# Kernel tuning notes

Measured on AMD Instinct MI355X. Metric: run time of the kernel, lower is better.

## Reference

```python
import jax, jax.numpy as jnp
import numpy as np

RADIUS = 0.12   # init_kwargs radius
NSAMPLE = 32    # init_kwargs nsample
USE_XYZ = True  # init_kwargs use_xyz


def ball_query(xyz, new_xyz, radius, nsample):
    """xyz: (B,N,3), new_xyz: (B,M,3) -> idx (B,M,nsample) int32.
    PointNet++ semantics: first `nsample` points (in index order) within
    `radius` of each query; slots past the count are padded with the first
    found index."""
    B, N, _ = xyz.shape
    # squared distances (B, M, N) -- the dominant intermediate
    d2 = jnp.sum((new_xyz[:, :, None, :] - xyz[:, None, :, :]) ** 2, axis=-1)
    mask = d2 < radius * radius
    # score so that earlier in-ball indices have higher score; out-of-ball = 0
    score = jnp.where(mask, (N - jnp.arange(N, dtype=jnp.int32)), 0)
    _, idx = jax.lax.top_k(score, nsample)            # (B, M, nsample)
    valid = jnp.take_along_axis(mask, idx, axis=-1)   # which slots are real hits
    idx = jnp.where(valid, idx, idx[..., :1])         # pad with first found index
    return idx


def group_points(feat, idx):
    """feat: (B,C,N), idx: (B,M,S) -> (B,C,M,S) gather along N."""
    B, C, N = feat.shape
    M, S = idx.shape[1], idx.shape[2]
    idx_flat = jnp.broadcast_to(idx.reshape(B, 1, M * S), (B, C, M * S))
    out = jnp.take_along_axis(feat, idx_flat, axis=2)
    return out.reshape(B, C, M, S)


def setup_inputs() -> dict:
    key = jax.random.key(0)
    k1, k2 = jax.random.split(key)
    B, N, M, C = 4, 8192, 4096, 64
    xyz = jax.random.uniform(k1, (B, N, 3), dtype=jnp.float32)  # points in unit cube
    new_xyz = xyz[:, :M, :]                                      # FPS-like subset of points
    features = jax.random.normal(k2, (B, C, N), dtype=jnp.float32)
    return {"xyz": xyz, "new_xyz": new_xyz, "features": features}


def reference(xyz, new_xyz, features):
    idx = ball_query(xyz, new_xyz, RADIUS, NSAMPLE)             # (B,M,S)
    xyz_t = jnp.transpose(xyz, (0, 2, 1))                        # (B,3,N)
    grouped_xyz = group_points(xyz_t, idx)                       # (B,3,M,S)
    grouped_xyz = grouped_xyz - jnp.transpose(new_xyz, (0, 2, 1))[..., None]
    grouped_feat = group_points(features, idx)                   # (B,C,M,S)
    if USE_XYZ:
        new_features = jnp.concatenate([grouped_xyz, grouped_feat], axis=1)
    else:
        new_features = grouped_feat
    return new_features  # (B, 3+C, M, S)
```

## Files before the change

kernel.cpp:

```cpp
#include <hip/hip_runtime.h>
#include <cstdint>
#include <cstddef>

#define BB 4
#define NN 8192
#define MM 4096
#define CC 64
#define SS 32
#define CH 67
#define NC 512
#define RMARG 0.1201f

__device__ __constant__ float kRR = (float)(0.12 * 0.12);

__device__ __forceinline__ int cell_of(float x, float y, float z) {
    const int ix = min((int)(x * 8.0f), 7);
    const int iy = min((int)(y * 8.0f), 7);
    const int iz = min((int)(z * 8.0f), 7);
    return (ix << 6) + (iy << 3) + iz;
}

__device__ __forceinline__ int block_scan512(int v, int tid, int* wsum) {
    int incl = v;
    #pragma unroll
    for (int d = 1; d < 64; d <<= 1) {
        const int t = __shfl_up(incl, d);
        if ((tid & 63) >= d) incl += t;
    }
    if ((tid & 63) == 63 && tid < NC) wsum[tid >> 6] = incl;
    __syncthreads();
    if (tid < 8) {
        const int ws = wsum[tid];
        int w2 = ws;
        #pragma unroll
        for (int d = 1; d < 8; d <<= 1) {
            const int t = __shfl_up(w2, d);
            if (tid >= d) w2 += t;
        }
        wsum[tid] = w2 - ws;
    }
    __syncthreads();
    return incl + wsum[(tid >> 6) & 7];
}

__global__ __launch_bounds__(1024) void k_prep(
    const float* __restrict__ xyz,
    const float* __restrict__ new_xyz,
    const float* __restrict__ feat,
    float* __restrict__ ft,
    int* __restrict__ cellStart,
    int* __restrict__ qperm,
    float4* __restrict__ pk)
{
    __shared__ __align__(16) char smem[64 * 65 * sizeof(float)];
    const int blk = (int)blockIdx.x;
    const int tid = (int)threadIdx.x;

    if (blk < BB) {
        int* sm   = (int*)smem;
        int* cur  = sm + NC;
        int* wsum = cur + NC;
        const int b = blk;

        if (tid < NC) sm[tid] = 0;
        __syncthreads();

        float xs[8], ys[8], zs[8];
        int cl[8];
        const float* __restrict__ xb = xyz + (size_t)b * NN * 3;
        #pragma unroll
        for (int k = 0; k < 8; ++k) {
            const int n = (k << 10) + tid;
            xs[k] = xb[n * 3 + 0];
            ys[k] = xb[n * 3 + 1];
            zs[k] = xb[n * 3 + 2];
            cl[k] = cell_of(xs[k], ys[k], zs[k]);
            atomicAdd(&sm[cl[k]], 1);
        }
        __syncthreads();

        const int v = (tid < NC) ? sm[tid] : 0;
        const int incl = block_scan512(v, tid, wsum);
        if (tid < NC) {
            cellStart[b * (NC + 1) + tid + 1] = incl;
            cur[tid] = incl - v;
            if (tid == 0) cellStart[b * (NC + 1)] = 0;
        }
        __syncthreads();

        #pragma unroll
        for (int k = 0; k < 8; ++k) {
            const int n = (k << 10) + tid;
            const int pos = atomicAdd(&cur[cl[k]], 1);
            pk[b * NN + pos] = make_float4(xs[k], ys[k], zs[k], __int_as_float(n));
        }
        __syncthreads();

        if (tid < NC) sm[tid] = 0;
        __syncthreads();
        int qcl[4];
        const float* __restrict__ qb = new_xyz + (size_t)b * MM * 3;
        #pragma unroll
        for (int k = 0; k < 4; ++k) {
            const int qm = (k << 10) + tid;
            const float qx = qb[qm * 3 + 0];
            const float qy = qb[qm * 3 + 1];
            const float qz = qb[qm * 3 + 2];
            qcl[k] = cell_of(qx, qy, qz);
            atomicAdd(&sm[qcl[k]], 1);
        }
        __syncthreads();
        const int qv = (tid < NC) ? sm[tid] : 0;
        const int qincl = block_scan512(qv, tid, wsum);
        if (tid < NC) cur[tid] = qincl - qv;
        __syncthreads();
        #pragma unroll
        for (int k = 0; k < 4; ++k) {
            const int qm = (k << 10) + tid;
            const int pos = atomicAdd(&cur[qcl[k]], 1);
            qperm[b * MM + pos] = qm;
        }
    } else {
        float (*tile)[65] = (float(*)[65])smem;
        const int blk2 = blk - BB;
        const int b = blk2 / (NN / 64);
        const int n0 = (blk2 % (NN / 64)) * 64;
        const int tn = tid & 63;
        const int q = tid >> 6;
        const float* __restrict__ fb = feat + (size_t)b * CC * NN;
        #pragma unroll
        for (int k = 0; k < 4; ++k) {
            const int c = (q << 2) + k;
            tile[tn][c] = fb[(size_t)c * NN + n0 + tn];
        }
        __syncthreads();
        float* fo = ft + ((size_t)b * NN + n0) * CC;
        #pragma unroll
        for (int k = 0; k < 4; ++k) {
            const int rn = (q << 2) + k;
            fo[(size_t)rn * CC + tn] = tile[rn][tn];
        }
    }
}

__global__ __launch_bounds__(256) void qg_grid_kernel(
    const float4* __restrict__ pk,
    const int* __restrict__ cellStart,
    const int* __restrict__ qperm,
    const float* __restrict__ ft,
    const float* __restrict__ xyz,
    const float* __restrict__ new_xyz,
    float* __restrict__ out)
{
    __shared__ unsigned int bm[4][NN / 32];
    __shared__ int slots_sm[4][SS];

    const int tid = (int)threadIdx.x;
    const int lane = tid & 63;
    const int w = tid >> 6;
    const int wave = (int)blockIdx.x * 4 + w;
    const int b = wave >> 12;
    const int msort = wave & (MM - 1);
    const int m = qperm[b * MM + msort];

    unsigned int* __restrict__ bitmap = bm[w];
    int* __restrict__ slot = slots_sm[w];

    #pragma unroll
    for (int k = 0; k < 4; ++k) bitmap[(k << 6) + lane] = 0u;

    const float* __restrict__ xb = xyz + (size_t)b * NN * 3;
    const size_t qoff = ((size_t)b * MM + m) * 3;
    const float cx = new_xyz[qoff + 0];
    const float cy = new_xyz[qoff + 1];
    const float cz = new_xyz[qoff + 2];
    const float rr = kRR;

    const int x0 = max(0, (int)((cx - RMARG) * 8.0f));
    const int x1 = min(7, (int)((cx + RMARG) * 8.0f));
    const int y0 = max(0, (int)((cy - RMARG) * 8.0f));
    const int y1 = min(7, (int)((cy + RMARG) * 8.0f));
    const int z0 = max(0, (int)((cz - RMARG) * 8.0f));
    const int z1 = min(7, (int)((cz + RMARG) * 8.0f));

    const int* __restrict__ cs = cellStart + b * (NC + 1);
    const float4* __restrict__ pb = pk + b * NN;

    const int ny = y1 - y0 + 1;
    const int npair = (x1 - x0 + 1) * ny;
    int begL = 0, endL = 0;
    if (lane < npair) {
        const int px = lane / ny;
        const int py = lane - px * ny;
        const int cb2 = ((x0 + px) << 6) + ((y0 + py) << 3);
        begL = cs[cb2 + z0];
        endL = cs[cb2 + z1 + 1];
    }

    for (int p = 0; p < npair; ++p) {
        const int beg = __shfl(begL, p);
        const int end = __shfl(endL, p);
        for (int off = beg; off < end; off += 64) {
            const int a = off + lane;
            const bool act = a < end;
            const float4 v = pb[act ? a : beg];
            const float dx = __fsub_rn(v.x, cx);
            const float dy = __fsub_rn(v.y, cy);
            const float dz = __fsub_rn(v.z, cz);
            const float d2 = __fadd_rn(__fadd_rn(__fmul_rn(dx, dx), __fmul_rn(dy, dy)),
                                       __fmul_rn(dz, dz));
            if (act && d2 < rr) {
                const int n = __float_as_int(v.w);
                atomicOr(&bitmap[n >> 5], 1u << (n & 31));
            }
        }
    }

    const uint4 wv = *reinterpret_cast<const uint4*>(&bitmap[lane << 2]);
    const int pc = __popc(wv.x) + __popc(wv.y) + __popc(wv.z) + __popc(wv.w);
    int incl = pc;
    #pragma unroll
    for (int d = 1; d < 64; d <<= 1) {
        const int t = __shfl_up(incl, d);
        if (lane >= d) incl += t;
    }
    const int K = __shfl(incl, 63);
    int r = incl - pc;
    if (r < SS) {
        const int base = lane << 7;
        unsigned int mw0 = wv.x, mw1 = wv.y, mw2 = wv.z, mw3 = wv.w;
        while (mw0 && r < SS) { slot[r++] = base +  0 + __builtin_ctz(mw0); mw0 &= mw0 - 1; }
        while (mw1 && r < SS) { slot[r++] = base + 32 + __builtin_ctz(mw1); mw1 &= mw1 - 1; }
        while (mw2 && r < SS) { slot[r++] = base + 64 + __builtin_ctz(mw2); mw2 &= mw2 - 1; }
        while (mw3 && r < SS) { slot[r++] = base + 96 + __builtin_ctz(mw3); mw3 &= mw3 - 1; }
    }

    const int s = lane & 31;
    const int h = lane >> 5;
    const int Kc = (K < SS) ? K : SS;
    int n_of;
    if (Kc == 0) n_of = 0;
    else n_of = (s < Kc) ? slot[s] : slot[0];

    const size_t obase = ((size_t)b * CH) * (size_t)(MM * SS) + (size_t)m * SS + s;

    if (h == 0) {
        const float* xr = xb + (size_t)n_of * 3;
        __builtin_nontemporal_store(__fsub_rn(xr[0], cx), &out[obase + 0 * (size_t)(MM * SS)]);
        __builtin_nontemporal_store(__fsub_rn(xr[1], cy), &out[obase + 1 * (size_t)(MM * SS)]);
        __builtin_nontemporal_store(__fsub_rn(xr[2], cz), &out[obase + 2 * (size_t)(MM * SS)]);
    }
    const float4* fr4 = (const float4*)(ft + ((size_t)b * NN + n_of) * CC + (h << 5));
    float4 f[8];
    #pragma unroll
    for (int j = 0; j < 8; ++j) f[j] = fr4[j];
    #pragma unroll
    for (int j = 0; j < 8; ++j) {
        float* cb = &out[obase + (size_t)(3 + (h << 5) + (j << 2)) * (size_t)(MM * SS)];
        __builtin_nontemporal_store(f[j].x, cb + 0 * (size_t)(MM * SS));
        __builtin_nontemporal_store(f[j].y, cb + 1 * (size_t)(MM * SS));
        __builtin_nontemporal_store(f[j].z, cb + 2 * (size_t)(MM * SS));
        __builtin_nontemporal_store(f[j].w, cb + 3 * (size_t)(MM * SS));
    }
}

__global__ __launch_bounds__(256) void qg_fused_kernel(
    const float* __restrict__ xyz, const float* __restrict__ new_xyz,
    const float* __restrict__ feat, float* __restrict__ out)
{
    const int wave = (int)((blockIdx.x * blockDim.x + threadIdx.x) >> 6);
    const int lane = (int)(threadIdx.x & 63);
    const int b = wave / MM;
    const int m = wave % MM;

    const float* __restrict__ xb = xyz + (size_t)b * NN * 3;
    const size_t qoff = ((size_t)b * MM + m) * 3;
    const float cx = new_xyz[qoff + 0];
    const float cy = new_xyz[qoff + 1];
    const float cz = new_xyz[qoff + 2];
    const float rr = kRR;

    int my_nb = -1;
    int cnt = 0;

    for (int base = 0; base < NN; base += 512) {
        float px[8], py[8], pz[8];
        #pragma unroll
        for (int k = 0; k < 8; ++k) {
            const int i = base + (k << 6) + lane;
            px[k] = xb[i * 3 + 0]; py[k] = xb[i * 3 + 1]; pz[k] = xb[i * 3 + 2];
        }
        #pragma unroll
        for (int k = 0; k < 8; ++k) {
            const float dx = __fsub_rn(px[k], cx);
            const float dy = __fsub_rn(py[k], cy);
            const float dz = __fsub_rn(pz[k], cz);
            const float d2 = __fadd_rn(__fadd_rn(__fmul_rn(dx, dx), __fmul_rn(dy, dy)),
                                       __fmul_rn(dz, dz));
            const bool hit = d2 < rr;
            const unsigned long long mask = __ballot(hit);
            const int pc = __popcll(mask);
            if (pc) {
                const int rank = cnt + (int)__popcll(mask & ((1ull << lane) - 1ull));
                const int addr = (hit && rank < 63) ? rank : 63;
                const int recv = __builtin_amdgcn_ds_permute(addr << 2,
                                                             base + (k << 6) + lane);
                if (lane >= cnt && lane < SS && (lane - cnt) < pc) my_nb = recv;
                cnt += pc;
                if (cnt >= SS) break;
            }
        }
        if (cnt >= SS) break;
    }

    int first = __shfl(my_nb, 0);
    if (first < 0) first = 0;
    if (lane < SS && my_nb < 0) my_nb = first;
    const int n_of = __shfl(my_nb, lane & 31);

    const int s = lane & 31;
    const int h = lane >> 5;
    const size_t obase = ((size_t)b * CH) * (size_t)(MM * SS) + (size_t)m * SS + s;
    const float* __restrict__ fb = feat + (size_t)b * CC * NN;
    #pragma unroll 2
    for (int cc = 0; cc < CH + 1; cc += 2) {
        const int c = cc + h;
        if (c < CH) {
            float v;
            if (c < 3) {
                const float center = (c == 0) ? cx : (c == 1) ? cy : cz;
                v = __fsub_rn(xb[(size_t)n_of * 3 + c], center);
            } else {
                v = fb[(size_t)(c - 3) * NN + n_of];
            }
            out[obase + (size_t)c * (size_t)(MM * SS)] = v;
        }
    }
}

extern "C" void kernel_launch(void* const* d_in, const int* in_sizes, int n_in,
                              void* d_out, int out_size, void* d_ws, size_t ws_size,
                              hipStream_t stream) {
    const float* xyz     = (const float*)d_in[0];
    const float* new_xyz = (const float*)d_in[1];
    const float* feat    = (const float*)d_in[2];
    float* out = (float*)d_out;

    const size_t ft_b = (size_t)BB * NN * CC * sizeof(float);
    float*  ft     = (float*)d_ws;
    int*    cellSt = (int*)((char*)d_ws + ft_b);
    int*    qperm  = cellSt + BB * (NC + 1);
    char*   after  = (char*)(qperm + BB * MM);
    float4* pk     = (float4*)(((uintptr_t)after + 15) & ~(uintptr_t)15);
    const size_t need = ((char*)(pk + BB * NN) - (char*)d_ws);

    if (ws_size >= need) {
        k_prep<<<BB + BB * (NN / 64), 1024, 0, stream>>>(xyz, new_xyz, feat, ft,
                                                         cellSt, qperm, pk);
        qg_grid_kernel<<<(BB * MM) / 4, 256, 0, stream>>>(pk, cellSt, qperm, ft,
                                                          xyz, new_xyz, out);
    } else {
        qg_fused_kernel<<<(BB * MM) / 4, 256, 0, stream>>>(xyz, new_xyz, feat, out);
    }
}
```

Baseline: 57.34 us.

## Process two consecutive queries per wave and drop query cell-sort permutation

Each wave now handles two adjacent queries in sequence, building a bitmap per query, then all 64 lanes write 64 contiguous output slots (two queries × 32 samples) per channel plane. This makes stores fully coalesced at 256 bytes per plane instead of 128. The qperm spatial sort of queries in the prep kernel is removed, so queries are processed in natural index order. The cost is half as many waves, each with serialized neighbor search, plus loss of spatial locality from the sort, which may increase divergence and cache misses.

```diff
diff --git a/kernel.cpp b/kernel.cpp
--- a/kernel.cpp
+++ b/kernel.cpp
@@ -45,11 +45,9 @@
 
 __global__ __launch_bounds__(1024) void k_prep(
     const float* __restrict__ xyz,
-    const float* __restrict__ new_xyz,
     const float* __restrict__ feat,
     float* __restrict__ ft,
     int* __restrict__ cellStart,
-    int* __restrict__ qperm,
     float4* __restrict__ pk)
 {
     __shared__ __align__(16) char smem[64 * 65 * sizeof(float)];
@@ -93,32 +91,6 @@
             const int n = (k << 10) + tid;
             const int pos = atomicAdd(&cur[cl[k]], 1);
             pk[b * NN + pos] = make_float4(xs[k], ys[k], zs[k], __int_as_float(n));
-        }
-        __syncthreads();
-
-        if (tid < NC) sm[tid] = 0;
-        __syncthreads();
-        int qcl[4];
-        const float* __restrict__ qb = new_xyz + (size_t)b * MM * 3;
-        #pragma unroll
-        for (int k = 0; k < 4; ++k) {
-            const int qm = (k << 10) + tid;
-            const float qx = qb[qm * 3 + 0];
-            const float qy = qb[qm * 3 + 1];
-            const float qz = qb[qm * 3 + 2];
-            qcl[k] = cell_of(qx, qy, qz);
-            atomicAdd(&sm[qcl[k]], 1);
-        }
-        __syncthreads();
-        const int qv = (tid < NC) ? sm[tid] : 0;
-        const int qincl = block_scan512(qv, tid, wsum);
-        if (tid < NC) cur[tid] = qincl - qv;
-        __syncthreads();
-        #pragma unroll
-        for (int k = 0; k < 4; ++k) {
-            const int qm = (k << 10) + tid;
-            const int pos = atomicAdd(&cur[qcl[k]], 1);
-            qperm[b * MM + pos] = qm;
         }
     } else {
         float (*tile)[65] = (float(*)[65])smem;
@@ -146,121 +118,133 @@
 __global__ __launch_bounds__(256) void qg_grid_kernel(
     const float4* __restrict__ pk,
     const int* __restrict__ cellStart,
-    const int* __restrict__ qperm,
     const float* __restrict__ ft,
     const float* __restrict__ xyz,
     const float* __restrict__ new_xyz,
     float* __restrict__ out)
 {
-    __shared__ unsigned int bm[4][NN / 32];
-    __shared__ int slots_sm[4][SS];
+    __shared__ unsigned int bm[4][2][NN / 32];
+    __shared__ int slots_sm[4][2][SS];
 
     const int tid = (int)threadIdx.x;
     const int lane = tid & 63;
     const int w = tid >> 6;
-    const int wave = (int)blockIdx.x * 4 + w;
-    const int b = wave >> 12;
-    const int msort = wave & (MM - 1);
-    const int m = qperm[b * MM + msort];
-
-    unsigned int* __restrict__ bitmap = bm[w];
-    int* __restrict__ slot = slots_sm[w];
+    const int pair = (int)blockIdx.x * 4 + w;
+    const int b = pair >> 11;
+    const int m0 = (pair & 2047) << 1;
 
     #pragma unroll
-    for (int k = 0; k < 4; ++k) bitmap[(k << 6) + lane] = 0u;
+    for (int k = 0; k < 8; ++k) bm[w][k & 1][((k >> 1) << 6) + lane] = 0u;
 
     const float* __restrict__ xb = xyz + (size_t)b * NN * 3;
-    const size_t qoff = ((size_t)b * MM + m) * 3;
-    const float cx = new_xyz[qoff + 0];
-    const float cy = new_xyz[qoff + 1];
-    const float cz = new_xyz[qoff + 2];
+    const float* __restrict__ qb = new_xyz + ((size_t)b * MM + m0) * 3;
+    const float cxq[2] = { qb[0], qb[3] };
+    const float cyq[2] = { qb[1], qb[4] };
+    const float czq[2] = { qb[2], qb[5] };
     const float rr = kRR;
-
-    const int x0 = max(0, (int)((cx - RMARG) * 8.0f));
-    const int x1 = min(7, (int)((cx + RMARG) * 8.0f));
-    const int y0 = max(0, (int)((cy - RMARG) * 8.0f));
-    const int y1 = min(7, (int)((cy + RMARG) * 8.0f));
-    const int z0 = max(0, (int)((cz - RMARG) * 8.0f));
-    const int z1 = min(7, (int)((cz + RMARG) * 8.0f));
 
     const int* __restrict__ cs = cellStart + b * (NC + 1);
     const float4* __restrict__ pb = pk + b * NN;
 
-    const int ny = y1 - y0 + 1;
-    const int npair = (x1 - x0 + 1) * ny;
-    int begL = 0, endL = 0;
-    if (lane < npair) {
-        const int px = lane / ny;
-        const int py = lane - px * ny;
-        const int cb2 = ((x0 + px) << 6) + ((y0 + py) << 3);
-        begL = cs[cb2 + z0];
-        endL = cs[cb2 + z1 + 1];
-    }
-
-    for (int p = 0; p < npair; ++p) {
-        const int beg = __shfl(begL, p);
-        const int end = __shfl(endL, p);
-        for (int off = beg; off < end; off += 64) {
-            const int a = off + lane;
-            const bool act = a < end;
-            const float4 v = pb[act ? a : beg];
-            const float dx = __fsub_rn(v.x, cx);
-            const float dy = __fsub_rn(v.y, cy);
-            const float dz = __fsub_rn(v.z, cz);
-            const float d2 = __fadd_rn(__fadd_rn(__fmul_rn(dx, dx), __fmul_rn(dy, dy)),
-                                       __fmul_rn(dz, dz));
-            if (act && d2 < rr) {
-                const int n = __float_as_int(v.w);
-                atomicOr(&bitmap[n >> 5], 1u << (n & 31));
+    int Kcq[2];
+
+    #pragma unroll
+    for (int q = 0; q < 2; ++q) {
+        const float cx = cxq[q], cy = cyq[q], cz = czq[q];
+        unsigned int* __restrict__ bitmap = bm[w][q];
+        int* __restrict__ slot = slots_sm[w][q];
+
+        const int x0 = max(0, (int)((cx - RMARG) * 8.0f));
+        const int x1 = min(7, (int)((cx + RMARG) * 8.0f));
+        const int y0 = max(0, (int)((cy - RMARG) * 8.0f));
+        const int y1 = min(7, (int)((cy + RMARG) * 8.0f));
+        const int z0 = max(0, (int)((cz - RMARG) * 8.0f));
+        const int z1 = min(7, (int)((cz + RMARG) * 8.0f));
+
+        const int ny = y1 - y0 + 1;
+        const int npair = (x1 - x0 + 1) * ny;
+        int begL = 0, endL = 0;
+        if (lane < npair) {
+            const int px = lane / ny;
+            const int py = lane - px * ny;
+            const int cb2 = ((x0 + px) << 6) + ((y0 + py) << 3);
+            begL = cs[cb2 + z0];
+            endL = cs[cb2 + z1 + 1];
+        }
+
+        for (int p = 0; p < npair; ++p) {
+            const int beg = __shfl(begL, p);
+            const int end = __shfl(endL, p);
+            for (int off = beg; off < end; off += 64) {
+                const int a = off + lane;
+                const bool act = a < end;
+                const float4 v = pb[act ? a : beg];
+                const float dx = __fsub_rn(v.x, cx);
+                const float dy = __fsub_rn(v.y, cy);
+                const float dz = __fsub_rn(v.z, cz);
+                const float d2 = __fadd_rn(__fadd_rn(__fmul_rn(dx, dx), __fmul_rn(dy, dy)),
+                                           __fmul_rn(dz, dz));
+                if (act && d2 < rr) {
+                    const int n = __float_as_int(v.w);
+                    atomicOr(&bitmap[n >> 5], 1u << (n & 31));
+                }
             }
         }
-    }
-
-    const uint4 wv = *reinterpret_cast<const uint4*>(&bitmap[lane << 2]);
-    const int pc = __popc(wv.x) + __popc(wv.y) + __popc(wv.z) + __popc(wv.w);
-    int incl = pc;
-    #pragma unroll
-    for (int d = 1; d < 64; d <<= 1) {
-        const int t = __shfl_up(incl, d);
-        if (lane >= d) incl += t;
-    }
-    const int K = __shfl(incl, 63);
-    int r = incl - pc;
-    if (r < SS) {
-        const int base = lane << 7;
-        unsigned int mw0 = wv.x, mw1 = wv.y, mw2 = wv.z, mw3 = wv.w;
-        while (mw0 && r < SS) { slot[r++] = base +  0 + __builtin_ctz(mw0); mw0 &= mw0 - 1; }
-        while (mw1 && r < SS) { slot[r++] = base + 32 + __builtin_ctz(mw1); mw1 &= mw1 - 1; }
-        while (mw2 && r < SS) { slot[r++] = base + 64 + __builtin_ctz(mw2); mw2 &= mw2 - 1; }
-        while (mw3 && r < SS) { slot[r++] = base + 96 + __builtin_ctz(mw3); mw3 &= mw3 - 1; }
-    }
-
+
+        const uint4 wv = *reinterpret_cast<const uint4*>(&bitmap[lane << 2]);
+        const int pc = __popc(wv.x) + __popc(wv.y) + __popc(wv.z) + __popc(wv.w);
+        int incl = pc;
+        #pragma unroll
+        for (int d = 1; d < 64; d <<= 1) {
+            const int t = __shfl_up(incl, d);
+            if (lane >= d) incl += t;
+        }
+        const int K = __shfl(incl, 63);
+        int r = incl - pc;
+        if (r < SS) {
+            const int base = lane << 7;
+            unsigned int mw0 = wv.x, mw1 = wv.y, mw2 = wv.z, mw3 = wv.w;
+            while (mw0 && r < SS) { slot[r++] = base +  0 + __builtin_ctz(mw0); mw0 &= mw0 - 1; }
+            while (mw1 && r < SS) { slot[r++] = base + 32 + __builtin_ctz(mw1); mw1 &= mw1 - 1; }
+            while (mw2 && r < SS) { slot[r++] = base + 64 + __builtin_ctz(mw2); mw2 &= mw2 - 1; }
+            while (mw3 && r < SS) { slot[r++] = base + 96 + __builtin_ctz(mw3); mw3 &= mw3 - 1; }
+        }
+        Kcq[q] = (K < SS) ? K : SS;
+    }
+
+    const int q = lane >> 5;
     const int s = lane & 31;
-    const int h = lane >> 5;
-    const int Kc = (K < SS) ? K : SS;
+    const int Kc = q ? Kcq[1] : Kcq[0];
     int n_of;
     if (Kc == 0) n_of = 0;
-    else n_of = (s < Kc) ? slot[s] : slot[0];
-
-    const size_t obase = ((size_t)b * CH) * (size_t)(MM * SS) + (size_t)m * SS + s;
-
-    if (h == 0) {
+    else n_of = slots_sm[w][q][(s < Kc) ? s : 0];
+
+    const size_t plane = (size_t)(MM * SS);
+    const size_t obase = ((size_t)b * CH) * plane + (size_t)m0 * SS + lane;
+
+    {
         const float* xr = xb + (size_t)n_of * 3;
-        __builtin_nontemporal_store(__fsub_rn(xr[0], cx), &out[obase + 0 * (size_t)(MM * SS)]);
-        __builtin_nontemporal_store(__fsub_rn(xr[1], cy), &out[obase + 1 * (size_t)(MM * SS)]);
-        __builtin_nontemporal_store(__fsub_rn(xr[2], cz), &out[obase + 2 * (size_t)(MM * SS)]);
-    }
-    const float4* fr4 = (const float4*)(ft + ((size_t)b * NN + n_of) * CC + (h << 5));
-    float4 f[8];
+        const float gx = __fsub_rn(xr[0], q ? cxq[1] : cxq[0]);
+        const float gy = __fsub_rn(xr[1], q ? cyq[1] : cyq[0]);
+        const float gz = __fsub_rn(xr[2], q ? czq[1] : czq[0]);
+        __builtin_nontemporal_store(gx, &out[obase + 0 * plane]);
+        __builtin_nontemporal_store(gy, &out[obase + 1 * plane]);
+        __builtin_nontemporal_store(gz, &out[obase + 2 * plane]);
+    }
+    const float4* fr4 = (const float4*)(ft + ((size_t)b * NN + n_of) * CC);
     #pragma unroll
-    for (int j = 0; j < 8; ++j) f[j] = fr4[j];
-    #pragma unroll
-    for (int j = 0; j < 8; ++j) {
-        float* cb = &out[obase + (size_t)(3 + (h << 5) + (j << 2)) * (size_t)(MM * SS)];
-        __builtin_nontemporal_store(f[j].x, cb + 0 * (size_t)(MM * SS));
-        __builtin_nontemporal_store(f[j].y, cb + 1 * (size_t)(MM * SS));
-        __builtin_nontemporal_store(f[j].z, cb + 2 * (size_t)(MM * SS));
-        __builtin_nontemporal_store(f[j].w, cb + 3 * (size_t)(MM * SS));
+    for (int half = 0; half < 2; ++half) {
+        float4 f[8];
+        #pragma unroll
+        for (int j = 0; j < 8; ++j) f[j] = fr4[(half << 3) + j];
+        #pragma unroll
+        for (int j = 0; j < 8; ++j) {
+            const int c0 = 3 + (half << 5) + (j << 2);
+            __builtin_nontemporal_store(f[j].x, &out[obase + (size_t)(c0 + 0) * plane]);
+            __builtin_nontemporal_store(f[j].y, &out[obase + (size_t)(c0 + 1) * plane]);
+            __builtin_nontemporal_store(f[j].z, &out[obase + (size_t)(c0 + 2) * plane]);
+            __builtin_nontemporal_store(f[j].w, &out[obase + (size_t)(c0 + 3) * plane]);
+        }
     }
 }
 
@@ -349,16 +333,14 @@
     const size_t ft_b = (size_t)BB * NN * CC * sizeof(float);
     float*  ft     = (float*)d_ws;
     int*    cellSt = (int*)((char*)d_ws + ft_b);
-    int*    qperm  = cellSt + BB * (NC + 1);
-    char*   after  = (char*)(qperm + BB * MM);
+    char*   after  = (char*)(cellSt + BB * (NC + 1));
     float4* pk     = (float4*)(((uintptr_t)after + 15) & ~(uintptr_t)15);
     const size_t need = ((char*)(pk + BB * NN) - (char*)d_ws);
 
     if (ws_size >= need) {
-        k_prep<<<BB + BB * (NN / 64), 1024, 0, stream>>>(xyz, new_xyz, feat, ft,
-                                                         cellSt, qperm, pk);
-        qg_grid_kernel<<<(BB * MM) / 4, 256, 0, stream>>>(pk, cellSt, qperm, ft,
-                                                          xyz, new_xyz, out);
+        k_prep<<<BB + BB * (NN / 64), 1024, 0, stream>>>(xyz, feat, ft, cellSt, pk);
+        qg_grid_kernel<<<(BB * MM) / 8, 256, 0, stream>>>(pk, cellSt, ft, xyz,
+                                                          new_xyz, out);
     } else {
         qg_fused_kernel<<<(BB * MM) / 4, 256, 0, stream>>>(xyz, new_xyz, feat, out);
     }
```

Result: slower. 59.21 us (+3.3%).
